# Optimization experiments

Measured on AMD Instinct MI355X. Metric: run time of the kernel, lower is better.

Reference implementation:

```python
import jax, jax.numpy as jnp
import numpy as np

HEADS = 8
BUCKET_SIZE = 128
KV_BUCKET_SIZE = 128
DIM = 64
TEMPERATURE = 0.7
SINKHORN_ITER = 8
EPS = 1e-6


def _log(t):
    # matches torch `log(t, eps=1e-6) = torch.log(t + eps)`
    return jnp.log(t + EPS)


def setup_inputs() -> dict:
    key = jax.random.key(0)
    k1, k2, k3 = jax.random.split(key, 3)
    q = jax.random.normal(k1, (32, 8192, 64), dtype=jnp.float32)
    k = jax.random.normal(k2, (32, 8192, 64), dtype=jnp.float32)
    # uniform sample used to build gumbel noise (deterministic substitute for
    # torch's in-module uniform_ sampling); shape == R shape [bh, buckets, kv_buckets]
    u_gumbel = jax.random.uniform(k3, (32, 64, 64), dtype=jnp.float32)
    return {"q": q, "k": k, "u_gumbel": u_gumbel, "topk": 1}


def reference(q, k, u_gumbel, topk):
    bh, q_len, dim = q.shape
    buckets = q_len // BUCKET_SIZE          # 64
    kv_buckets = k.shape[1] // KV_BUCKET_SIZE  # 64

    # bucket then mean over bucket contents -> [bh, buckets, dim]
    sq = q.reshape(bh, buckets, BUCKET_SIZE, dim).mean(axis=2)
    sk = k.reshape(bh, kv_buckets, KV_BUCKET_SIZE, dim).mean(axis=2)

    # bucket-to-bucket similarity [bh, buckets, kv_buckets]
    R = jnp.einsum('bie,bje->bij', sq, sk) * (DIM ** -0.5)

    # gumbel_sinkhorn(F.relu(R), sinkhorn_iter, temperature)
    r = _log(jax.nn.relu(R))
    gumbel = -_log(-_log(u_gumbel))
    r = (r + gumbel) / TEMPERATURE

    # sinkhorn normalization: alternate col/row log-space normalization
    for _ in range(SINKHORN_ITER):
        r = r - jax.scipy.special.logsumexp(r, axis=2, keepdims=True)
        r = r - jax.scipy.special.logsumexp(r, axis=1, keepdims=True)
    return jnp.exp(r)
```

## Files before the change

### kernel.cpp

```cpp
#include <hip/hip_runtime.h>
#include <hip/hip_bf16.h>
#include <math.h>

#define EPSF 1e-6f

typedef float float4n __attribute__((ext_vector_type(4)));

__device__ inline float readlane_f(float v, int l) {
    return __int_as_float(__builtin_amdgcn_readlane(__float_as_int(v), l));
}

__global__ __launch_bounds__(256) void bucket_mean_kernel(
    const float* __restrict__ q,
    const float* __restrict__ k,
    float* __restrict__ sqk)
{
    int g      = blockIdx.x * 4 + (threadIdx.x >> 6);
    int t      = g >> 11;
    int bh     = (g >> 6) & 31;
    int bucket = g & 63;

    const float* src = t ? k : q;
    const float4n* base = reinterpret_cast<const float4n*>(
        src + ((size_t)bh * 8192 + (size_t)bucket * 128) * 64);

    int lane = threadIdx.x & 63;
    int rr   = lane >> 4;
    int c    = lane & 15;

    float4n acc = (float4n)(0.f);
    #pragma unroll
    for (int b = 0; b < 2; ++b) {
        float4n v[16];
        #pragma unroll
        for (int u = 0; u < 16; ++u)
            v[u] = __builtin_nontemporal_load(&base[(rr + (b * 16 + u) * 4) * 16 + c]);
        #pragma unroll
        for (int u = 0; u < 16; ++u)
            acc += v[u];
    }

    acc.x += __shfl_xor(acc.x, 16, 64);
    acc.y += __shfl_xor(acc.y, 16, 64);
    acc.z += __shfl_xor(acc.z, 16, 64);
    acc.w += __shfl_xor(acc.w, 16, 64);
    acc.x += __shfl_xor(acc.x, 32, 64);
    acc.y += __shfl_xor(acc.y, 32, 64);
    acc.z += __shfl_xor(acc.z, 32, 64);
    acc.w += __shfl_xor(acc.w, 32, 64);

    if (lane < 16) {
        acc *= (1.0f / 128.0f);
        float4n* dst = reinterpret_cast<float4n*>(
            sqk + (size_t)t * 32 * 64 * 64 + ((size_t)bh * 64 + bucket) * 64);
        dst[c] = acc;
    }
}

__global__ __launch_bounds__(1024) void sinkhorn_kernel(
    const float* __restrict__ sqk,
    const float* __restrict__ u_gumbel,
    float* __restrict__ out)
{
    int bh  = blockIdx.x;
    int tid = threadIdx.x;

    __shared__ float sk_s[64][65];
    __shared__ float r_s[64][65];

    const float* sqp = sqk + (size_t)bh * 4096;
    const float* skp = sqk + (size_t)32 * 4096 + (size_t)bh * 4096;

    #pragma unroll
    for (int t = 0; t < 4; ++t) {
        int idx = tid + 1024 * t;
        sk_s[idx >> 6][idx & 63] = skp[idx];
    }

    int lane = tid & 63;
    int i0   = tid >> 6;

    float sqr0 = sqp[(i0     ) * 64 + lane];
    float sqr1 = sqp[(i0 + 16) * 64 + lane];
    float sqr2 = sqp[(i0 + 32) * 64 + lane];
    float sqr3 = sqp[(i0 + 48) * 64 + lane];
    __syncthreads();

    {
        int j = lane;
        float acc0 = 0.f, acc1 = 0.f, acc2 = 0.f, acc3 = 0.f;
        #pragma unroll
        for (int e = 0; e < 64; ++e) {
            float s = sk_s[j][e];
            acc0 = fmaf(readlane_f(sqr0, e), s, acc0);
            acc1 = fmaf(readlane_f(sqr1, e), s, acc1);
            acc2 = fmaf(readlane_f(sqr2, e), s, acc2);
            acc3 = fmaf(readlane_f(sqr3, e), s, acc3);
        }
        const float scale = 0.125f;
        const float invT  = 1.0f / 0.7f;
        float accs[4] = {acc0, acc1, acc2, acc3};
        #pragma unroll
        for (int t = 0; t < 4; ++t) {
            int i   = i0 + 16 * t;
            float R = accs[t] * scale;
            float rl = fmaxf(R, 0.f);
            float u  = u_gumbel[(size_t)bh * 4096 + i * 64 + j];
            float gm = -__logf(-__logf(u + EPSF) + EPSF);
            r_s[i][j] = (__logf(rl + EPSF) + gm) * invT;
        }
    }
    __syncthreads();

    int lane16 = tid & 15;
    int rc     = tid >> 4;
    int cbase  = lane16 * 4;
    for (int it = 0; it < 8; ++it) {
        {
            float v0 = r_s[rc][cbase + 0], v1 = r_s[rc][cbase + 1];
            float v2 = r_s[rc][cbase + 2], v3 = r_s[rc][cbase + 3];
            float m = fmaxf(fmaxf(v0, v1), fmaxf(v2, v3));
            m = fmaxf(m, __shfl_xor(m, 1, 64));
            m = fmaxf(m, __shfl_xor(m, 2, 64));
            m = fmaxf(m, __shfl_xor(m, 4, 64));
            m = fmaxf(m, __shfl_xor(m, 8, 64));
            float s = __expf(v0 - m) + __expf(v1 - m)
                    + __expf(v2 - m) + __expf(v3 - m);
            s += __shfl_xor(s, 1, 64);
            s += __shfl_xor(s, 2, 64);
            s += __shfl_xor(s, 4, 64);
            s += __shfl_xor(s, 8, 64);
            float lse = m + __logf(s);
            r_s[rc][cbase + 0] = v0 - lse;
            r_s[rc][cbase + 1] = v1 - lse;
            r_s[rc][cbase + 2] = v2 - lse;
            r_s[rc][cbase + 3] = v3 - lse;
        }
        __syncthreads();
        {
            float v0 = r_s[cbase + 0][rc], v1 = r_s[cbase + 1][rc];
            float v2 = r_s[cbase + 2][rc], v3 = r_s[cbase + 3][rc];
            float m = fmaxf(fmaxf(v0, v1), fmaxf(v2, v3));
            m = fmaxf(m, __shfl_xor(m, 1, 64));
            m = fmaxf(m, __shfl_xor(m, 2, 64));
            m = fmaxf(m, __shfl_xor(m, 4, 64));
            m = fmaxf(m, __shfl_xor(m, 8, 64));
            float s = __expf(v0 - m) + __expf(v1 - m)
                    + __expf(v2 - m) + __expf(v3 - m);
            s += __shfl_xor(s, 1, 64);
            s += __shfl_xor(s, 2, 64);
            s += __shfl_xor(s, 4, 64);
            s += __shfl_xor(s, 8, 64);
            float lse = m + __logf(s);
            r_s[cbase + 0][rc] = v0 - lse;
            r_s[cbase + 1][rc] = v1 - lse;
            r_s[cbase + 2][rc] = v2 - lse;
            r_s[cbase + 3][rc] = v3 - lse;
        }
        __syncthreads();
    }

    #pragma unroll
    for (int t = 0; t < 4; ++t) {
        int idx = tid + 1024 * t;
        out[(size_t)bh * 4096 + idx] = __expf(r_s[idx >> 6][idx & 63]);
    }
}

extern "C" void kernel_launch(void* const* d_in, const int* in_sizes, int n_in,
                              void* d_out, int out_size, void* d_ws, size_t ws_size,
                              hipStream_t stream) {
    const float* q = (const float*)d_in[0];
    const float* k = (const float*)d_in[1];
    const float* u = (const float*)d_in[2];
    float* out = (float*)d_out;
    float* sqk = (float*)d_ws;

    bucket_mean_kernel<<<1024, 256, 0, stream>>>(q, k, sqk);
    sinkhorn_kernel<<<32, 1024, 0, stream>>>(sqk, u, out);
}
```

Baseline: 158.3 us.

## Run Sinkhorn in linear space on one wavefront with register-resident columns

The log-space Sinkhorn loop, with its logsumexp and max reductions and block-wide barriers each half-iteration, is replaced by linear-space normalization. The matrix is exponentiated once, then a single 64-lane wavefront keeps one column per lane in registers. Row sums use cross-lane shuffles, column sums are in-register, and both scale by hardware reciprocals. This removes the transcendental calls and the repeated __syncthreads in the loop. In exchange, 960 of the 1024 threads sit idle, the reduction chain is serialized across 64 rows, and linear-space values may lose precision or overflow for extreme gumbel samples.

New measurement: 184.6 us. 16.6% more time.

```diff
diff --git a/kernel.cpp b/kernel.cpp
--- a/kernel.cpp
+++ b/kernel.cpp
@@ -66,7 +66,7 @@
     int tid = threadIdx.x;
 
     __shared__ float sk_s[64][65];
-    __shared__ float r_s[64][65];
+    __shared__ float s_s[64][65];
 
     const float* sqp = sqk + (size_t)bh * 4096;
     const float* skp = sqk + (size_t)32 * 4096 + (size_t)bh * 4096;
@@ -103,67 +103,51 @@
         #pragma unroll
         for (int t = 0; t < 4; ++t) {
             int i   = i0 + 16 * t;
-            float R = accs[t] * scale;
-            float rl = fmaxf(R, 0.f);
+            float rl = fmaxf(accs[t] * scale, 0.f);
             float u  = u_gumbel[(size_t)bh * 4096 + i * 64 + j];
             float gm = -__logf(-__logf(u + EPSF) + EPSF);
-            r_s[i][j] = (__logf(rl + EPSF) + gm) * invT;
+            s_s[i][j] = __expf((__logf(rl + EPSF) + gm) * invT);
         }
     }
     __syncthreads();
 
-    int lane16 = tid & 15;
-    int rc     = tid >> 4;
-    int cbase  = lane16 * 4;
-    for (int it = 0; it < 8; ++it) {
-        {
-            float v0 = r_s[rc][cbase + 0], v1 = r_s[rc][cbase + 1];
-            float v2 = r_s[rc][cbase + 2], v3 = r_s[rc][cbase + 3];
-            float m = fmaxf(fmaxf(v0, v1), fmaxf(v2, v3));
-            m = fmaxf(m, __shfl_xor(m, 1, 64));
-            m = fmaxf(m, __shfl_xor(m, 2, 64));
-            m = fmaxf(m, __shfl_xor(m, 4, 64));
-            m = fmaxf(m, __shfl_xor(m, 8, 64));
-            float s = __expf(v0 - m) + __expf(v1 - m)
-                    + __expf(v2 - m) + __expf(v3 - m);
-            s += __shfl_xor(s, 1, 64);
-            s += __shfl_xor(s, 2, 64);
-            s += __shfl_xor(s, 4, 64);
-            s += __shfl_xor(s, 8, 64);
-            float lse = m + __logf(s);
-            r_s[rc][cbase + 0] = v0 - lse;
-            r_s[rc][cbase + 1] = v1 - lse;
-            r_s[rc][cbase + 2] = v2 - lse;
-            r_s[rc][cbase + 3] = v3 - lse;
+    if (tid < 64) {
+        float s[64];
+        #pragma unroll
+        for (int i = 0; i < 64; ++i) s[i] = s_s[i][tid];
+
+        #pragma unroll 1
+        for (int it = 0; it < 8; ++it) {
+            #pragma unroll
+            for (int i = 0; i < 64; ++i) {
+                float t = s[i];
+                t += __shfl_xor(t, 1, 64);
+                t += __shfl_xor(t, 2, 64);
+                t += __shfl_xor(t, 4, 64);
+                t += __shfl_xor(t, 8, 64);
+                t += __shfl_xor(t, 16, 64);
+                t += __shfl_xor(t, 32, 64);
+                s[i] *= __builtin_amdgcn_rcpf(t);
+            }
+            float t0 = 0.f, t1 = 0.f, t2 = 0.f, t3 = 0.f;
+            #pragma unroll
+            for (int i = 0; i < 64; i += 4) {
+                t0 += s[i]; t1 += s[i + 1]; t2 += s[i + 2]; t3 += s[i + 3];
+            }
+            float rc = __builtin_amdgcn_rcpf((t0 + t1) + (t2 + t3));
+            #pragma unroll
+            for (int i = 0; i < 64; ++i) s[i] *= rc;
         }
-        __syncthreads();
-        {
-            float v0 = r_s[cbase + 0][rc], v1 = r_s[cbase + 1][rc];
-            float v2 = r_s[cbase + 2][rc], v3 = r_s[cbase + 3][rc];
-            float m = fmaxf(fmaxf(v0, v1), fmaxf(v2, v3));
-            m = fmaxf(m, __shfl_xor(m, 1, 64));
-            m = fmaxf(m, __shfl_xor(m, 2, 64));
-            m = fmaxf(m, __shfl_xor(m, 4, 64));
-            m = fmaxf(m, __shfl_xor(m, 8, 64));
-            float s = __expf(v0 - m) + __expf(v1 - m)
-                    + __expf(v2 - m) + __expf(v3 - m);
-            s += __shfl_xor(s, 1, 64);
-            s += __shfl_xor(s, 2, 64);
-            s += __shfl_xor(s, 4, 64);
-            s += __shfl_xor(s, 8, 64);
-            float lse = m + __logf(s);
-            r_s[cbase + 0][rc] = v0 - lse;
-            r_s[cbase + 1][rc] = v1 - lse;
-            r_s[cbase + 2][rc] = v2 - lse;
-            r_s[cbase + 3][rc] = v3 - lse;
-        }
-        __syncthreads();
+
+        #pragma unroll
+        for (int i = 0; i < 64; ++i) s_s[i][tid] = s[i];
     }
+    __syncthreads();
 
     #pragma unroll
     for (int t = 0; t < 4; ++t) {
         int idx = tid + 1024 * t;
-        out[(size_t)bh * 4096 + idx] = __expf(r_s[idx >> 6][idx & 63]);
+        out[(size_t)bh * 4096 + idx] = s_s[idx >> 6][idx & 63];
     }
 }
 
```
